# Optimization experiments

Hardware: AMD Instinct MI355X
Metric: run time of the kernel (lower is better)

## Reference

```python
import jax, jax.numpy as jnp
import numpy as np

WINDOW = 21
PATCH = 1
H_PARAM = 0.1
EPS = 1e-10


def _box_sum(x, w):
    # Sum over a w x w sliding window (VALID), per (batch, channel).
    return jax.lax.reduce_window(x, 0.0, jax.lax.add,
                                 (1, 1, w, w), (1, 1, 1, 1), 'VALID')


def setup_inputs() -> dict:
    key = jax.random.key(0)
    noisy = jax.random.uniform(key, (8, 3, 512, 512), dtype=jnp.float32)
    return {"noisy": noisy}


def reference(noisy) -> jnp.ndarray:
    # Faithful vectorization of the per-pixel loop for patch_size=1.
    # For each pixel p=(i,j):
    #   window = padded[i:i+W, j:j+W]; center = noisy[i,j]
    #   dists  = mean((window - center)^2)
    #   weights = exp(-dists / h^2)            # shape (B, C)
    #   patch  = window[0, 0] = padded[i, j]   # top-left of window (half_patch=0)
    #   out[:, c, i, j] = sum_b weights[b,c] * patch[b,c]   (sum over BATCH)
    #   wsum[:, c, i, j] = sum_b weights[b,c]
    # out = clamp(out / (wsum + 1e-10), 0, 1)
    h2 = H_PARAM * H_PARAM
    W = WINDOW
    pad = W // 2
    B, C, Hh, Ww = noisy.shape
    padded = jnp.pad(noisy, ((0, 0), (0, 0), (pad, pad), (pad, pad)), mode='reflect')

    # mean((window - center)^2) = (S2 - 2*center*S1 + W^2*center^2) / W^2
    s1 = _box_sum(padded, W)                  # (B, C, H, W)
    s2 = _box_sum(padded * padded, W)
    n_win = jnp.asarray(W * W, dtype=noisy.dtype)
    dists = (s2 - 2.0 * noisy * s1 + n_win * noisy * noisy) / n_win

    weights = jnp.exp(-dists / h2)            # (B, C, H, W)
    patch = padded[:, :, :Hh, :Ww]            # top-left pixel of each window

    num = jnp.sum(weights * patch, axis=0, keepdims=True)   # (1, C, H, W)
    den = jnp.sum(weights, axis=0, keepdims=True)
    out = num / (den + EPS)
    out = jnp.broadcast_to(out, noisy.shape)  # loop assigns same row to all b
    return jnp.clip(out, 0.0, 1.0)
```

## Files before the change

### kernel.cpp

```cpp
#include <hip/hip_runtime.h>

#define B 8
#define CCH 3
#define HH 512
#define WW 512
#define WIN 21
#define PAD 10
#define TSX 32
#define TSY 32
#define PTY 52
#define TROW 60
#define HSH 53
#define NSLOT 676

__global__ __launch_bounds__(256, 3) void nlm_fused_kernel(const float* __restrict__ noisy,
                                                           float* __restrict__ out) {
    __shared__ float  tile[PTY][TROW];
    __shared__ float2 hs_t[TSX][HSH];

    const int tid = threadIdx.x;
    const int x0 = blockIdx.x * TSX;
    const int y0 = blockIdx.y * TSY;
    const int ch = blockIdx.z;

    int   rowbase[3], gxs[3];
    float* ldsp[3];
    bool  valid[3], edge[3];
    #pragma unroll
    for (int k = 0; k < 3; ++k) {
        int s = tid + 256 * k;
        valid[k] = (s < NSLOT);
        int ss = valid[k] ? s : 0;
        int r  = ss / 13;
        int c4 = ss - r * 13;
        int gy = y0 + r - PAD;
        gy = (gy < 0) ? -gy : ((gy >= HH) ? (2 * (HH - 1) - gy) : gy);
        int gx = x0 + (c4 << 2) - PAD;
        rowbase[k] = gy * WW;
        gxs[k]     = gx;
        edge[k]    = (gx < 0) || (gx > WW - 4);
        ldsp[k]    = &tile[r][c4 << 2];
    }

    const float* src0 = noisy + (size_t)ch * (HH * WW);
    float4 pre[3];
    #pragma unroll
    for (int k = 0; k < 3; ++k) {
        if (valid[k]) {
            if (!edge[k]) {
                pre[k] = *(const float4*)(src0 + rowbase[k] + gxs[k]);
            } else {
                float tmp[4];
                #pragma unroll
                for (int t = 0; t < 4; ++t) {
                    int gx = gxs[k] + t;
                    gx = (gx < 0) ? -gx : ((gx >= WW) ? (2 * (WW - 1) - gx) : gx);
                    tmp[t] = src0[rowbase[k] + gx];
                }
                pre[k] = make_float4(tmp[0], tmp[1], tmp[2], tmp[3]);
            }
        }
    }

    float num[4] = {0.f, 0.f, 0.f, 0.f};
    float den[4] = {0.f, 0.f, 0.f, 0.f};

    const int tx  = tid & 31;
    const int ty0 = (tid >> 5) << 2;

    for (int b = 0; b < B; ++b) {
        __syncthreads();
        #pragma unroll
        for (int k = 0; k < 3; ++k)
            if (valid[k]) *(float4*)ldsp[k] = pre[k];
        __syncthreads();

        if (b < B - 1) {
            const float* srcn = noisy + (size_t)((b + 1) * CCH + ch) * (HH * WW);
            #pragma unroll
            for (int k = 0; k < 3; ++k) {
                if (valid[k]) {
                    if (!edge[k]) {
                        pre[k] = *(const float4*)(srcn + rowbase[k] + gxs[k]);
                    } else {
                        float tmp[4];
                        #pragma unroll
                        for (int t = 0; t < 4; ++t) {
                            int gx = gxs[k] + t;
                            gx = (gx < 0) ? -gx : ((gx >= WW) ? (2 * (WW - 1) - gx) : gx);
                            tmp[t] = srcn[rowbase[k] + gx];
                        }
                        pre[k] = make_float4(tmp[0], tmp[1], tmp[2], tmp[3]);
                    }
                }
            }
        }

        if (tid < PTY * 4) {
            int r   = tid >> 2;
            int cx0 = (tid & 3) << 3;
            float v[28];
            #pragma unroll
            for (int q = 0; q < 7; ++q)
                *(float4*)&v[q * 4] = *(const float4*)&tile[r][cx0 + (q << 2)];
            float s1 = 0.f, s2 = 0.f;
            #pragma unroll
            for (int k = 0; k <= 20; ++k) { s1 += v[k]; s2 = fmaf(v[k], v[k], s2); }
            hs_t[cx0][r] = make_float2(s1, s2);
            #pragma unroll
            for (int j = 1; j < 8; ++j) {
                float vo = v[j - 1], vn = v[j + 20];
                s1 += vn - vo;
                s2 += vn * vn - vo * vo;
                hs_t[cx0 + j][r] = make_float2(s1, s2);
            }
        }
        __syncthreads();

        float2 h0 = hs_t[tx][ty0];
        float2 h1 = hs_t[tx][ty0 + 1];
        float2 h2 = hs_t[tx][ty0 + 2];
        float vs1 = h0.x + h1.x + h2.x;
        float vs2 = h0.y + h1.y + h2.y;
        #pragma unroll
        for (int k = 3; k <= 20; ++k) {
            float2 h = hs_t[tx][ty0 + k];
            vs1 += h.x;
            vs2 += h.y;
        }
        const float kE = (-100.0f / 441.0f) * 1.44269504088896f;
        {
            float a = tile[ty0 + PAD][tx + PAD];
            float p = tile[ty0][tx];
            float dd = fmaf(a, fmaf(441.f, a, -2.f * vs1), vs2);
            float w = exp2f(dd * kE);
            num[0] += w * p; den[0] += w;
        }
        #pragma unroll
        for (int i = 1; i < 4; ++i) {
            float2 hn = hs_t[tx][ty0 + 20 + i];
            float2 ho = (i == 1) ? h0 : ((i == 2) ? h1 : h2);
            vs1 += hn.x - ho.x;
            vs2 += hn.y - ho.y;
            float a = tile[ty0 + i + PAD][tx + PAD];
            float p = tile[ty0 + i][tx];
            float dd = fmaf(a, fmaf(441.f, a, -2.f * vs1), vs2);
            float w = exp2f(dd * kE);
            num[i] += w * p; den[i] += w;
        }
    }

    #pragma unroll
    for (int i = 0; i < 4; ++i) {
        int y = y0 + ty0 + i;
        int x = x0 + tx;
        float v = num[i] / (den[i] + 1e-10f);
        v = v < 0.f ? 0.f : (v > 1.f ? 1.f : v);
        #pragma unroll
        for (int b = 0; b < B; ++b)
            out[((size_t)(b * CCH + ch) * HH + y) * WW + x] = v;
    }
}

extern "C" void kernel_launch(void* const* d_in, const int* in_sizes, int n_in,
                              void* d_out, int out_size, void* d_ws, size_t ws_size,
                              hipStream_t stream) {
    const float* noisy = (const float*)d_in[0];
    float* out = (float*)d_out;
    dim3 grid(WW / TSX, HH / TSY, CCH);
    nlm_fused_kernel<<<grid, dim3(256), 0, stream>>>(noisy, out);
}
```

Measured before the change: 88.94 us.

## Split batch accumulation across two block groups with a finalize kernel

```diff
diff --git a/kernel.cpp b/kernel.cpp
--- a/kernel.cpp
+++ b/kernel.cpp
@@ -1,6 +1,8 @@
 #include <hip/hip_runtime.h>
 
 #define B 8
+#define NG 2
+#define GB 4
 #define CCH 3
 #define HH 512
 #define WW 512
@@ -12,16 +14,18 @@
 #define TROW 60
 #define HSH 53
 #define NSLOT 676
-
-__global__ __launch_bounds__(256, 3) void nlm_fused_kernel(const float* __restrict__ noisy,
-                                                           float* __restrict__ out) {
+#define NPIX (CCH * HH * WW)
+
+__global__ __launch_bounds__(256, 6) void nlm_accum_kernel(const float* __restrict__ noisy,
+                                                           float2* __restrict__ ws) {
     __shared__ float  tile[PTY][TROW];
     __shared__ float2 hs_t[TSX][HSH];
 
     const int tid = threadIdx.x;
     const int x0 = blockIdx.x * TSX;
     const int y0 = blockIdx.y * TSY;
-    const int ch = blockIdx.z;
+    const int ch = blockIdx.z % CCH;
+    const int g  = blockIdx.z / CCH;
 
     int   rowbase[3], gxs[3];
     float* ldsp[3];
@@ -42,7 +46,7 @@
         ldsp[k]    = &tile[r][c4 << 2];
     }
 
-    const float* src0 = noisy + (size_t)ch * (HH * WW);
+    const float* src0 = noisy + (size_t)(g * GB * CCH + ch) * (HH * WW);
     float4 pre[3];
     #pragma unroll
     for (int k = 0; k < 3; ++k) {
@@ -68,15 +72,15 @@
     const int tx  = tid & 31;
     const int ty0 = (tid >> 5) << 2;
 
-    for (int b = 0; b < B; ++b) {
+    for (int lb = 0; lb < GB; ++lb) {
         __syncthreads();
         #pragma unroll
         for (int k = 0; k < 3; ++k)
             if (valid[k]) *(float4*)ldsp[k] = pre[k];
         __syncthreads();
 
-        if (b < B - 1) {
-            const float* srcn = noisy + (size_t)((b + 1) * CCH + ch) * (HH * WW);
+        if (lb < GB - 1) {
+            const float* srcn = noisy + (size_t)((g * GB + lb + 1) * CCH + ch) * (HH * WW);
             #pragma unroll
             for (int k = 0; k < 3; ++k) {
                 if (valid[k]) {
@@ -150,16 +154,36 @@
         }
     }
 
+    float2* wsg = ws + (size_t)g * NPIX;
     #pragma unroll
     for (int i = 0; i < 4; ++i) {
         int y = y0 + ty0 + i;
         int x = x0 + tx;
-        float v = num[i] / (den[i] + 1e-10f);
-        v = v < 0.f ? 0.f : (v > 1.f ? 1.f : v);
-        #pragma unroll
-        for (int b = 0; b < B; ++b)
-            out[((size_t)(b * CCH + ch) * HH + y) * WW + x] = v;
-    }
+        wsg[((size_t)ch * HH + y) * WW + x] = make_float2(num[i], den[i]);
+    }
+}
+
+__global__ __launch_bounds__(256) void nlm_finalize_kernel(const float* __restrict__ ws,
+                                                           float* __restrict__ out) {
+    int i4 = (blockIdx.x * 256 + threadIdx.x) << 2;
+    const float* g0 = ws + ((size_t)i4 << 1);
+    const float* g1 = g0 + ((size_t)NPIX << 1);
+    float4 a0 = *(const float4*)g0;
+    float4 a1 = *(const float4*)(g0 + 4);
+    float4 b0 = *(const float4*)g1;
+    float4 b1 = *(const float4*)(g1 + 4);
+    float4 v;
+    v.x = (a0.x + b0.x) / (a0.y + b0.y + 1e-10f);
+    v.y = (a0.z + b0.z) / (a0.w + b0.w + 1e-10f);
+    v.z = (a1.x + b1.x) / (a1.y + b1.y + 1e-10f);
+    v.w = (a1.z + b1.z) / (a1.w + b1.w + 1e-10f);
+    v.x = v.x < 0.f ? 0.f : (v.x > 1.f ? 1.f : v.x);
+    v.y = v.y < 0.f ? 0.f : (v.y > 1.f ? 1.f : v.y);
+    v.z = v.z < 0.f ? 0.f : (v.z > 1.f ? 1.f : v.z);
+    v.w = v.w < 0.f ? 0.f : (v.w > 1.f ? 1.f : v.w);
+    #pragma unroll
+    for (int b = 0; b < B; ++b)
+        *(float4*)(out + (size_t)b * NPIX + i4) = v;
 }
 
 extern "C" void kernel_launch(void* const* d_in, const int* in_sizes, int n_in,
@@ -167,6 +191,11 @@
                               hipStream_t stream) {
     const float* noisy = (const float*)d_in[0];
     float* out = (float*)d_out;
-    dim3 grid(WW / TSX, HH / TSY, CCH);
-    nlm_fused_kernel<<<grid, dim3(256), 0, stream>>>(noisy, out);
+    float2* ws = (float2*)d_ws;
+
+    dim3 grid1(WW / TSX, HH / TSY, CCH * NG);
+    nlm_accum_kernel<<<grid1, dim3(256), 0, stream>>>(noisy, ws);
+
+    dim3 grid2(NPIX / (256 * 4));
+    nlm_finalize_kernel<<<grid2, dim3(256), 0, stream>>>((const float*)d_ws, out);
 }
```

Result: slower. 179.8 us (+102.2%).

## Double-buffer LDS tile and row-sum arrays to cut per-batch barriers

Applied to the files above, without the earlier changes.

```diff
diff --git a/kernel.cpp b/kernel.cpp
--- a/kernel.cpp
+++ b/kernel.cpp
@@ -15,16 +15,15 @@
 
 __global__ __launch_bounds__(256, 3) void nlm_fused_kernel(const float* __restrict__ noisy,
                                                            float* __restrict__ out) {
-    __shared__ float  tile[PTY][TROW];
-    __shared__ float2 hs_t[TSX][HSH];
+    __shared__ float  tile[2][PTY][TROW];
+    __shared__ float2 hs_t[2][TSX][HSH];
 
     const int tid = threadIdx.x;
     const int x0 = blockIdx.x * TSX;
     const int y0 = blockIdx.y * TSY;
     const int ch = blockIdx.z;
 
-    int   rowbase[3], gxs[3];
-    float* ldsp[3];
+    int   rowbase[3], gxs[3], lr[3], lc[3];
     bool  valid[3], edge[3];
     #pragma unroll
     for (int k = 0; k < 3; ++k) {
@@ -39,115 +38,107 @@
         rowbase[k] = gy * WW;
         gxs[k]     = gx;
         edge[k]    = (gx < 0) || (gx > WW - 4);
-        ldsp[k]    = &tile[r][c4 << 2];
+        lr[k]      = r;
+        lc[k]      = c4 << 2;
     }
 
-    const float* src0 = noisy + (size_t)ch * (HH * WW);
     float4 pre[3];
-    #pragma unroll
-    for (int k = 0; k < 3; ++k) {
-        if (valid[k]) {
-            if (!edge[k]) {
-                pre[k] = *(const float4*)(src0 + rowbase[k] + gxs[k]);
-            } else {
-                float tmp[4];
-                #pragma unroll
-                for (int t = 0; t < 4; ++t) {
-                    int gx = gxs[k] + t;
-                    gx = (gx < 0) ? -gx : ((gx >= WW) ? (2 * (WW - 1) - gx) : gx);
-                    tmp[t] = src0[rowbase[k] + gx];
+    auto prefetch = [&](int bb) {
+        const float* src = noisy + (size_t)(bb * CCH + ch) * (HH * WW);
+        #pragma unroll
+        for (int k = 0; k < 3; ++k) {
+            if (valid[k]) {
+                if (!edge[k]) {
+                    pre[k] = *(const float4*)(src + rowbase[k] + gxs[k]);
+                } else {
+                    float tmp[4];
+                    #pragma unroll
+                    for (int t = 0; t < 4; ++t) {
+                        int gx = gxs[k] + t;
+                        gx = (gx < 0) ? -gx : ((gx >= WW) ? (2 * (WW - 1) - gx) : gx);
+                        tmp[t] = src[rowbase[k] + gx];
+                    }
+                    pre[k] = make_float4(tmp[0], tmp[1], tmp[2], tmp[3]);
                 }
-                pre[k] = make_float4(tmp[0], tmp[1], tmp[2], tmp[3]);
             }
         }
-    }
+    };
+
+    prefetch(0);
+    #pragma unroll
+    for (int k = 0; k < 3; ++k)
+        if (valid[k]) *(float4*)&tile[0][lr[k]][lc[k]] = pre[k];
+    prefetch(1);
+    __syncthreads();
 
     float num[4] = {0.f, 0.f, 0.f, 0.f};
     float den[4] = {0.f, 0.f, 0.f, 0.f};
 
     const int tx  = tid & 31;
     const int ty0 = (tid >> 5) << 2;
+    const int hr  = tid >> 2;
+    const int hc0 = (tid & 3) << 3;
 
     for (int b = 0; b < B; ++b) {
-        __syncthreads();
-        #pragma unroll
-        for (int k = 0; k < 3; ++k)
-            if (valid[k]) *(float4*)ldsp[k] = pre[k];
-        __syncthreads();
-
-        if (b < B - 1) {
-            const float* srcn = noisy + (size_t)((b + 1) * CCH + ch) * (HH * WW);
-            #pragma unroll
-            for (int k = 0; k < 3; ++k) {
-                if (valid[k]) {
-                    if (!edge[k]) {
-                        pre[k] = *(const float4*)(srcn + rowbase[k] + gxs[k]);
-                    } else {
-                        float tmp[4];
-                        #pragma unroll
-                        for (int t = 0; t < 4; ++t) {
-                            int gx = gxs[k] + t;
-                            gx = (gx < 0) ? -gx : ((gx >= WW) ? (2 * (WW - 1) - gx) : gx);
-                            tmp[t] = srcn[rowbase[k] + gx];
-                        }
-                        pre[k] = make_float4(tmp[0], tmp[1], tmp[2], tmp[3]);
-                    }
-                }
-            }
-        }
-
-        if (tid < PTY * 4) {
-            int r   = tid >> 2;
-            int cx0 = (tid & 3) << 3;
+        const int cur = b & 1;
+        if (hr < PTY) {
             float v[28];
             #pragma unroll
             for (int q = 0; q < 7; ++q)
-                *(float4*)&v[q * 4] = *(const float4*)&tile[r][cx0 + (q << 2)];
+                *(float4*)&v[q * 4] = *(const float4*)&tile[cur][hr][hc0 + (q << 2)];
             float s1 = 0.f, s2 = 0.f;
             #pragma unroll
             for (int k = 0; k <= 20; ++k) { s1 += v[k]; s2 = fmaf(v[k], v[k], s2); }
-            hs_t[cx0][r] = make_float2(s1, s2);
+            hs_t[cur][hc0][hr] = make_float2(s1, s2);
             #pragma unroll
             for (int j = 1; j < 8; ++j) {
                 float vo = v[j - 1], vn = v[j + 20];
                 s1 += vn - vo;
                 s2 += vn * vn - vo * vo;
-                hs_t[cx0 + j][r] = make_float2(s1, s2);
+                hs_t[cur][hc0 + j][hr] = make_float2(s1, s2);
             }
         }
         __syncthreads();
 
-        float2 h0 = hs_t[tx][ty0];
-        float2 h1 = hs_t[tx][ty0 + 1];
-        float2 h2 = hs_t[tx][ty0 + 2];
+        if (b < B - 1) {
+            #pragma unroll
+            for (int k = 0; k < 3; ++k)
+                if (valid[k]) *(float4*)&tile[1 - cur][lr[k]][lc[k]] = pre[k];
+            if (b < B - 2) prefetch(b + 2);
+        }
+
+        float2 h0 = hs_t[cur][tx][ty0];
+        float2 h1 = hs_t[cur][tx][ty0 + 1];
+        float2 h2 = hs_t[cur][tx][ty0 + 2];
         float vs1 = h0.x + h1.x + h2.x;
         float vs2 = h0.y + h1.y + h2.y;
         #pragma unroll
         for (int k = 3; k <= 20; ++k) {
-            float2 h = hs_t[tx][ty0 + k];
+            float2 h = hs_t[cur][tx][ty0 + k];
             vs1 += h.x;
             vs2 += h.y;
         }
         const float kE = (-100.0f / 441.0f) * 1.44269504088896f;
         {
-            float a = tile[ty0 + PAD][tx + PAD];
-            float p = tile[ty0][tx];
+            float a = tile[cur][ty0 + PAD][tx + PAD];
+            float p = tile[cur][ty0][tx];
             float dd = fmaf(a, fmaf(441.f, a, -2.f * vs1), vs2);
             float w = exp2f(dd * kE);
             num[0] += w * p; den[0] += w;
         }
         #pragma unroll
         for (int i = 1; i < 4; ++i) {
-            float2 hn = hs_t[tx][ty0 + 20 + i];
+            float2 hn = hs_t[cur][tx][ty0 + 20 + i];
             float2 ho = (i == 1) ? h0 : ((i == 2) ? h1 : h2);
             vs1 += hn.x - ho.x;
             vs2 += hn.y - ho.y;
-            float a = tile[ty0 + i + PAD][tx + PAD];
-            float p = tile[ty0 + i][tx];
+            float a = tile[cur][ty0 + i + PAD][tx + PAD];
+            float p = tile[cur][ty0 + i][tx];
             float dd = fmaf(a, fmaf(441.f, a, -2.f * vs1), vs2);
             float w = exp2f(dd * kE);
             num[i] += w * p; den[i] += w;
         }
+        if (b < B - 1) __syncthreads();
     }
 
     #pragma unroll
```

New measurement: 90.55 us. About the same (+1.8%).
